# Kernel tuning notes

Measured on AMD Instinct MI355X. Metric: run time of the kernel, lower is better.

## Reference

```python
import jax, jax.numpy as jnp
import numpy as np

NEG_SLOPE = 0.2  # PyG GATConv LeakyReLU slope
HEADS = 4

def _gat_conv(x, edge_index, W, a_src, a_dst, b):
    """Single-relation GATConv (PyG semantics, concat=True).
    x: [N, Fin]; edge_index: [2, E]; W: [Fin, H*D]; a_src/a_dst: [H, D]; b: [H*D].
    """
    N = x.shape[0]
    H, D = a_src.shape
    h = (x @ W).reshape(N, H, D)                      # [N, H, D]
    src, dst = edge_index[0], edge_index[1]
    # per-node attention halves
    al_s = jnp.einsum('nhd,hd->nh', h, a_src)         # [N, H]
    al_d = jnp.einsum('nhd,hd->nh', h, a_dst)         # [N, H]
    alpha = jax.nn.leaky_relu(al_s[src] + al_d[dst], NEG_SLOPE)  # [E, H]
    # segment softmax over incoming edges per destination node
    amax = jax.ops.segment_max(alpha, dst, num_segments=N)       # [N, H]
    e = jnp.exp(alpha - amax[dst])
    denom = jax.ops.segment_sum(e, dst, num_segments=N)          # [N, H]
    w = e / (denom[dst] + 1e-16)                                  # [E, H]
    msg = h[src] * w[:, :, None]                                  # [E, H, D]
    out = jax.ops.segment_sum(msg, dst, num_segments=N)          # [N, H, D]
    return out.reshape(N, H * D) + b

def setup_inputs() -> dict:
    key = jax.random.key(0)
    ks = jax.random.split(key, 8)
    N, Fin, Fout, E, R = 50000, 256, 128, 800000, 3
    return {
        'x': jax.random.normal(ks[0], (N, Fin), dtype=jnp.float32),
        'edge_index_0': jax.random.randint(ks[1], (2, E), 0, N, dtype=jnp.int32),
        'edge_index_1': jax.random.randint(ks[2], (2, E), 0, N, dtype=jnp.int32),
        'edge_index_2': jax.random.randint(ks[3], (2, E), 0, N, dtype=jnp.int32),
        'W': jax.random.normal(ks[4], (R, Fin, Fout), dtype=jnp.float32) * 0.05,
        'att_src': jax.random.normal(ks[5], (R, HEADS, Fout // HEADS), dtype=jnp.float32) * 0.1,
        'att_dst': jax.random.normal(ks[6], (R, HEADS, Fout // HEADS), dtype=jnp.float32) * 0.1,
        'bias': jax.random.normal(ks[7], (R, Fout), dtype=jnp.float32) * 0.01,
    }

def reference(x, edge_index_0, edge_index_1, edge_index_2, W, att_src, att_dst, bias):
    edges = (edge_index_0, edge_index_1, edge_index_2)
    out = None
    for r in range(W.shape[0]):  # small fixed relation loop
        h_rel = _gat_conv(x, edges[r], W[r], att_src[r], att_dst[r], bias[r])
        out = h_rel if out is None else out + h_rel
    return out
```

## Files before the change

kernel.cpp:

```cpp
#include <hip/hip_runtime.h>
#include <hip/hip_bf16.h>

#define NEG_SLOPE 0.2f
#define NBMAX 320
#define KB    512
#define CAP   10240
#define CHUNK 4096

typedef short bf16x8 __attribute__((ext_vector_type(8)));
typedef float f32x4  __attribute__((ext_vector_type(4)));
typedef float f32x16 __attribute__((ext_vector_type(16)));

__device__ inline ushort f2bf(float f) {
  __hip_bfloat16 b = __float2bfloat16(f);
  return *(ushort*)&b;
}

__global__ __launch_bounds__(256)
void prep_kernel(const float* __restrict__ W,
                 const float* __restrict__ a_src,
                 const float* __restrict__ a_dst,
                 ushort* __restrict__ WbigT,
                 int* __restrict__ bcnt) {
  const int b = blockIdx.x;
  const int t = threadIdx.x;
  if (b == 448) {
    for (int k = t; k < NBMAX; k += 256) bcnt[k] = 0;
    return;
  }
  int i = b * 256 + t;
  int c = i >> 8, k = i & 255;
  float v = 0.f;
  if (c < 384) {
    int r = c >> 7, j = c & 127;
    v = W[((size_t)r * 256 + k) * 128 + j];
  } else if (c < 408) {
    int c6 = c - 384, r = c6 >> 3, hh = c6 & 7, hd = hh & 3;
    const float* a = (hh < 4 ? a_src : a_dst) + (r * 4 + hd) * 32;
    const float* wp = W + ((size_t)r * 256 + k) * 128 + hd * 32;
#pragma unroll
    for (int d = 0; d < 32; ++d) v += wp[d] * a[d];
  }
  WbigT[i] = f2bf(v);
}

__device__ inline void edge_decode(int i, int E0, int E1,
                                   const int* __restrict__ s0, const int* __restrict__ d0,
                                   const int* __restrict__ s1, const int* __restrict__ d1,
                                   const int* __restrict__ s2, const int* __restrict__ d2,
                                   int N, int& src, int& key) {
  if (i < E0)            { src = s0[i];            key = d0[i]; }
  else if (i < E0 + E1)  { src = s1[i - E0];       key = N + d1[i - E0]; }
  else                   { src = s2[i - E0 - E1];  key = 2 * N + d2[i - E0 - E1]; }
}

struct GemmSmem {
  ushort As[64][40];
  ushort Bs[448][40];
};
struct StageSmem {
  ushort es_src[CHUNK];
  int    es_key[CHUNK];
  int    lh[NBMAX];
  int    lb[NBMAX];
};

__global__ __launch_bounds__(256, 2)
void gemm_stage_kernel(const float* __restrict__ x, const ushort* __restrict__ WT,
                       ushort* __restrict__ hall, float* __restrict__ al, int M,
                       const int* __restrict__ s0, const int* __restrict__ d0,
                       const int* __restrict__ s1, const int* __restrict__ d1,
                       const int* __restrict__ s2, const int* __restrict__ d2,
                       int E0, int E1, int E2,
                       int* __restrict__ bcnt, unsigned* __restrict__ staging,
                       int N, int NB, int GB) {
  __shared__ __align__(16) char smem_raw[sizeof(GemmSmem) > sizeof(StageSmem)
                                             ? sizeof(GemmSmem) : sizeof(StageSmem)];
  const int t = threadIdx.x;

  if (blockIdx.x < GB) {
    GemmSmem& sm = *reinterpret_cast<GemmSmem*>(smem_raw);
    const int bm = blockIdx.x * 64;
    const int l = t & 63;
    const int w = t >> 6;
    const int wm = (w >> 1) * 32;
    const int wn = (w & 1) * 224;
    const int lr31 = l & 31;
    const int kg = (l >> 5) * 8;

    f32x16 acc[7];
#pragma unroll
    for (int j = 0; j < 7; ++j)
#pragma unroll
      for (int r = 0; r < 16; ++r) acc[j][r] = 0.f;

    for (int k0 = 0; k0 < 256; k0 += 32) {
      {
        int row = t >> 2, seg = t & 3;
        int grow = bm + row;
        float4 v0 = make_float4(0.f, 0.f, 0.f, 0.f), v1 = v0;
        if (grow < M) {
          const float* xp = x + (size_t)grow * 256 + k0 + seg * 8;
          v0 = *(const float4*)xp;
          v1 = *(const float4*)(xp + 4);
        }
        uint4 pk;
        pk.x = (unsigned)f2bf(v0.x) | ((unsigned)f2bf(v0.y) << 16);
        pk.y = (unsigned)f2bf(v0.z) | ((unsigned)f2bf(v0.w) << 16);
        pk.z = (unsigned)f2bf(v1.x) | ((unsigned)f2bf(v1.y) << 16);
        pk.w = (unsigned)f2bf(v1.z) | ((unsigned)f2bf(v1.w) << 16);
        *(uint4*)&sm.As[row][seg * 8] = pk;
      }
#pragma unroll
      for (int p = 0; p < 7; ++p) {
        int idx = p * 256 + t;
        int nrow = idx >> 2, ch = idx & 3;
        *(uint4*)&sm.Bs[nrow][ch * 8] =
            *(const uint4*)(WT + (size_t)nrow * 256 + k0 + ch * 8);
      }
      __syncthreads();
#pragma unroll
      for (int kk = 0; kk < 32; kk += 16) {
        bf16x8 af = *(bf16x8*)&sm.As[wm + lr31][kk + kg];
#pragma unroll
        for (int j = 0; j < 7; ++j) {
          bf16x8 bf = *(bf16x8*)&sm.Bs[wn + j * 32 + lr31][kk + kg];
          acc[j] = __builtin_amdgcn_mfma_f32_32x32x16_bf16(af, bf, acc[j], 0, 0, 0);
        }
      }
      __syncthreads();
    }

#pragma unroll
    for (int j = 0; j < 7; ++j) {
      int gcol = wn + j * 32 + lr31;
#pragma unroll
      for (int r = 0; r < 16; ++r) {
        int grow = bm + wm + (l >> 5) * 4 + (r & 3) + 8 * (r >> 2);
        if (grow >= M) continue;
        float c = acc[j][r];
        if (gcol < 384) {
          int rel = gcol >> 7, jj = gcol & 127;
          hall[((size_t)rel * M + grow) * 128 + jj] = f2bf(c);
        } else if (gcol < 408) {
          int c6 = gcol - 384, rr = c6 >> 3, hh = c6 & 7;
          al[(((size_t)(hh < 4 ? 0 : 3) + rr) * M + grow) * 4 + (hh & 3)] = c;
        }
      }
    }
  } else {
    StageSmem& sm = *reinterpret_cast<StageSmem*>(smem_raw);
    for (int k = t; k < NB; k += 256) sm.lh[k] = 0;
    __syncthreads();
    const int Etot = E0 + E1 + E2;
    const int lo = (blockIdx.x - GB) * CHUNK;
    const int hi = min(lo + CHUNK, Etot);
    const int n = hi - lo;
    for (int i = t; i < n; i += 256) {
      int src, key;
      edge_decode(lo + i, E0, E1, s0, d0, s1, d1, s2, d2, N, src, key);
      sm.es_src[i] = (ushort)src;
      sm.es_key[i] = key;
      atomicAdd(&sm.lh[key >> 9], 1);
    }
    __syncthreads();
    for (int k = t; k < NB; k += 256) {
      int v = sm.lh[k];
      sm.lb[k] = v ? (k * CAP + atomicAdd(&bcnt[k], v)) : 0;
      sm.lh[k] = 0;
    }
    __syncthreads();
    for (int i = t; i < n; i += 256) {
      int key = sm.es_key[i];
      int b = key >> 9;
      int pos = sm.lb[b] + atomicAdd(&sm.lh[b], 1);
      if (pos < (b + 1) * CAP)
        staging[pos] = ((unsigned)(key & 511) << 16) | (unsigned)sm.es_src[i];
    }
  }
}

__global__ __launch_bounds__(512)
void bucket_sort(const unsigned* __restrict__ staging, const int* __restrict__ bcnt,
                 int* __restrict__ offs, int* __restrict__ ends,
                 ushort* __restrict__ srt, int n3) {
  __shared__ int cnt[KB];
  __shared__ int cur[KB];
  __shared__ int wsum[8];
  const int b = blockIdx.x;
  const int base = b * KB;
  const int lo = b * CAP;
  const int t = threadIdx.x;
  const int lane = t & 63, wid = t >> 6;
  const int m = min(bcnt[b], CAP);
  cnt[t] = 0;
  __syncthreads();
  for (int i = t; i < m; i += 512)
    atomicAdd(&cnt[staging[lo + i] >> 16], 1);
  __syncthreads();
  int v = cnt[t];
  int sv = v;
#pragma unroll
  for (int d = 1; d < 64; d <<= 1) {
    int u = __shfl_up(sv, d);
    if (lane >= d) sv += u;
  }
  if (lane == 63) wsum[wid] = sv;
  __syncthreads();
  if (t < 8) {
    int ws = wsum[t];
#pragma unroll
    for (int d = 1; d < 8; d <<= 1) {
      int u = __shfl_up(ws, d);
      if (t >= d) ws += u;
    }
    wsum[t] = ws;
  }
  __syncthreads();
  int start = lo + (wid ? wsum[wid - 1] : 0) + sv - v;
  cur[t] = start;
  if (base + t < n3) {
    offs[base + t] = start;
    ends[base + t] = start + v;
  }
  __syncthreads();
  for (int i = t; i < m; i += 512) {
    unsigned p = staging[lo + i];
    int pos = atomicAdd(&cur[p >> 16], 1);
    srt[pos] = (ushort)(p & 0xffffu);
  }
}

__global__ __launch_bounds__(128)
void gat_fused_kernel(const ushort* __restrict__ srt, const int* __restrict__ offs,
                      const int* __restrict__ ends,
                      const ushort* __restrict__ hall,
                      const float* __restrict__ al,
                      const float* __restrict__ bias,
                      float* __restrict__ out, int N) {
  const int d = blockIdx.x;
  const int t = threadIdx.x;
  const int w = t >> 6;
  const int l = t & 63;
  const int eg = l >> 4;
  const int fl = l & 15;
  const int h = fl >> 2;

  __shared__ float slab[3][2][16][9];

#pragma unroll
  for (int rel = 0; rel < 3; ++rel) {
    const int key = rel * N + d;
    const int start = offs[key];
    const int dend = ends[key];
    const float* alS = al + (size_t)rel * N * 4;
    const ushort* hrel = hall + (size_t)rel * N * 128;
    const float ald = al[((size_t)(3 + rel) * N + d) * 4 + h];
    float r0 = 0.f, r1 = 0.f, r2 = 0.f, r3 = 0.f;
    float r4 = 0.f, r5 = 0.f, r6 = 0.f, r7 = 0.f;
    float dl = 0.f;
#pragma unroll 2
    for (int e = start + w * 4 + eg; e < dend; e += 8) {
      int s = srt[e];
      float a = alS[(size_t)s * 4 + h] + ald;
      a = fmaxf(a, NEG_SLOPE * a);
      float ex = __expf(a);
      dl += ex;
      uint4 u = *(const uint4*)(hrel + (size_t)s * 128 + fl * 8);
      r0 += __uint_as_float(u.x << 16) * ex;
      r1 += __uint_as_float(u.x & 0xffff0000u) * ex;
      r2 += __uint_as_float(u.y << 16) * ex;
      r3 += __uint_as_float(u.y & 0xffff0000u) * ex;
      r4 += __uint_as_float(u.z << 16) * ex;
      r5 += __uint_as_float(u.z & 0xffff0000u) * ex;
      r6 += __uint_as_float(u.w << 16) * ex;
      r7 += __uint_as_float(u.w & 0xffff0000u) * ex;
    }
    r0 += __shfl_xor(r0, 16); r0 += __shfl_xor(r0, 32);
    r1 += __shfl_xor(r1, 16); r1 += __shfl_xor(r1, 32);
    r2 += __shfl_xor(r2, 16); r2 += __shfl_xor(r2, 32);
    r3 += __shfl_xor(r3, 16); r3 += __shfl_xor(r3, 32);
    r4 += __shfl_xor(r4, 16); r4 += __shfl_xor(r4, 32);
    r5 += __shfl_xor(r5, 16); r5 += __shfl_xor(r5, 32);
    r6 += __shfl_xor(r6, 16); r6 += __shfl_xor(r6, 32);
    r7 += __shfl_xor(r7, 16); r7 += __shfl_xor(r7, 32);
    dl += __shfl_xor(dl, 16); dl += __shfl_xor(dl, 32);
    if (l < 16) {
      slab[rel][w][fl][0] = r0; slab[rel][w][fl][1] = r1;
      slab[rel][w][fl][2] = r2; slab[rel][w][fl][3] = r3;
      slab[rel][w][fl][4] = r4; slab[rel][w][fl][5] = r5;
      slab[rel][w][fl][6] = r6; slab[rel][w][fl][7] = r7;
      slab[rel][w][fl][8] = dl;
    }
  }
  __syncthreads();
  {
    int fl2 = t >> 3, k = t & 7;
    int f = fl2 * 8 + k;
    float o = bias[f] + bias[128 + f] + bias[256 + f];
#pragma unroll
    for (int rel = 0; rel < 3; ++rel) {
      float D = slab[rel][0][fl2][8] + slab[rel][1][fl2][8];
      float R = slab[rel][0][fl2][k] + slab[rel][1][fl2][k];
      o += R / (D + 1e-16f);
    }
    out[(size_t)d * 128 + f] = o;
  }
}

extern "C" void kernel_launch(void* const* d_in, const int* in_sizes, int n_in,
                              void* d_out, int out_size, void* d_ws, size_t ws_size,
                              hipStream_t stream) {
  const float* x     = (const float*)d_in[0];
  const int*   ei[3] = {(const int*)d_in[1], (const int*)d_in[2], (const int*)d_in[3]};
  const float* W     = (const float*)d_in[4];
  const float* a_src = (const float*)d_in[5];
  const float* a_dst = (const float*)d_in[6];
  const float* bias  = (const float*)d_in[7];

  const int Fin = 256;
  const int N = in_sizes[0] / Fin;
  const int E0 = in_sizes[1] / 2, E1 = in_sizes[2] / 2, E2 = in_sizes[3] / 2;
  const int Etot = E0 + E1 + E2;
  const int n3 = 3 * N;
  const int NB = (n3 + KB - 1) / KB;
  const int GB = (N + 63) / 64;
  const int SB = (Etot + CHUNK - 1) / CHUNK;

  float* out = (float*)d_out;

  char* p = (char*)d_ws;
  ushort*   WbigT   = (ushort*)p;    p += (size_t)448 * 256 * 2;
  ushort*   hall    = (ushort*)p;    p += (size_t)N * 384 * 2;
  float*    al      = (float*)p;     p += (size_t)6 * N * 4 * 4;
  unsigned* staging = (unsigned*)p;  p += (size_t)NBMAX * CAP * 4;
  ushort*   srt     = (ushort*)p;    p += (size_t)NBMAX * CAP * 2;
  int*      offs    = (int*)p;       p += (size_t)n3 * 4;
  int*      ends    = (int*)p;       p += (size_t)n3 * 4;
  int*      bcnt    = (int*)p;       p += NBMAX * 4;

  prep_kernel<<<449, 256, 0, stream>>>(W, a_src, a_dst, WbigT, bcnt);

  gemm_stage_kernel<<<GB + SB, 256, 0, stream>>>(
      x, WbigT, hall, al, N,
      ei[0], ei[0] + E0, ei[1], ei[1] + E1, ei[2], ei[2] + E2,
      E0, E1, E2, bcnt, staging, N, NB, GB);

  bucket_sort<<<NB, 512, 0, stream>>>(staging, bcnt, offs, ends, srt, n3);

  gat_fused_kernel<<<N, 128, 0, stream>>>(srt, offs, ends, hall, al, bias, out, N);
}
```

Baseline: 199.6 us.

## Regroup kernels: fuse edge staging with weight prep, bucket sort with GEMM

After: 198.9 us (median of 2 runs). Within noise of the previous version (-0.4%).

```diff
diff --git a/kernel.cpp b/kernel.cpp
--- a/kernel.cpp
+++ b/kernel.cpp
@@ -8,40 +8,11 @@
 #define CHUNK 4096
 
 typedef short bf16x8 __attribute__((ext_vector_type(8)));
-typedef float f32x4  __attribute__((ext_vector_type(4)));
 typedef float f32x16 __attribute__((ext_vector_type(16)));
 
 __device__ inline ushort f2bf(float f) {
   __hip_bfloat16 b = __float2bfloat16(f);
   return *(ushort*)&b;
-}
-
-__global__ __launch_bounds__(256)
-void prep_kernel(const float* __restrict__ W,
-                 const float* __restrict__ a_src,
-                 const float* __restrict__ a_dst,
-                 ushort* __restrict__ WbigT,
-                 int* __restrict__ bcnt) {
-  const int b = blockIdx.x;
-  const int t = threadIdx.x;
-  if (b == 448) {
-    for (int k = t; k < NBMAX; k += 256) bcnt[k] = 0;
-    return;
-  }
-  int i = b * 256 + t;
-  int c = i >> 8, k = i & 255;
-  float v = 0.f;
-  if (c < 384) {
-    int r = c >> 7, j = c & 127;
-    v = W[((size_t)r * 256 + k) * 128 + j];
-  } else if (c < 408) {
-    int c6 = c - 384, r = c6 >> 3, hh = c6 & 7, hd = hh & 3;
-    const float* a = (hh < 4 ? a_src : a_dst) + (r * 4 + hd) * 32;
-    const float* wp = W + ((size_t)r * 256 + k) * 128 + hd * 32;
-#pragma unroll
-    for (int d = 0; d < 32; ++d) v += wp[d] * a[d];
-  }
-  WbigT[i] = f2bf(v);
 }
 
 __device__ inline void edge_decode(int i, int E0, int E1,
@@ -54,10 +25,6 @@
   else                   { src = s2[i - E0 - E1];  key = 2 * N + d2[i - E0 - E1]; }
 }
 
-struct GemmSmem {
-  ushort As[64][40];
-  ushort Bs[448][40];
-};
 struct StageSmem {
   ushort es_src[CHUNK];
   int    es_key[CHUNK];
@@ -66,21 +33,144 @@
 };
 
 __global__ __launch_bounds__(256, 2)
-void gemm_stage_kernel(const float* __restrict__ x, const ushort* __restrict__ WT,
-                       ushort* __restrict__ hall, float* __restrict__ al, int M,
-                       const int* __restrict__ s0, const int* __restrict__ d0,
+void stage_prep_kernel(const int* __restrict__ s0, const int* __restrict__ d0,
                        const int* __restrict__ s1, const int* __restrict__ d1,
                        const int* __restrict__ s2, const int* __restrict__ d2,
                        int E0, int E1, int E2,
                        int* __restrict__ bcnt, unsigned* __restrict__ staging,
-                       int N, int NB, int GB) {
-  __shared__ __align__(16) char smem_raw[sizeof(GemmSmem) > sizeof(StageSmem)
-                                             ? sizeof(GemmSmem) : sizeof(StageSmem)];
+                       int N, int NB, int SB,
+                       const float* __restrict__ W,
+                       const float* __restrict__ a_src,
+                       const float* __restrict__ a_dst,
+                       ushort* __restrict__ WbigT) {
+  __shared__ __align__(16) char smem_raw[sizeof(StageSmem)];
   const int t = threadIdx.x;
-
-  if (blockIdx.x < GB) {
+  if (blockIdx.x >= SB) {
+    int i = (blockIdx.x - SB) * 256 + t;
+    int c = i >> 8, k = i & 255;
+    float v = 0.f;
+    if (c < 384) {
+      int r = c >> 7, j = c & 127;
+      v = W[((size_t)r * 256 + k) * 128 + j];
+    } else if (c < 408) {
+      int c6 = c - 384, r = c6 >> 3, hh = c6 & 7, hd = hh & 3;
+      const float* a = (hh < 4 ? a_src : a_dst) + (r * 4 + hd) * 32;
+      const float* wp = W + ((size_t)r * 256 + k) * 128 + hd * 32;
+#pragma unroll
+      for (int d = 0; d < 32; ++d) v += wp[d] * a[d];
+    }
+    WbigT[i] = f2bf(v);
+    return;
+  }
+  StageSmem& sm = *reinterpret_cast<StageSmem*>(smem_raw);
+  for (int k = t; k < NB; k += 256) sm.lh[k] = 0;
+  __syncthreads();
+  const int Etot = E0 + E1 + E2;
+  const int lo = blockIdx.x * CHUNK;
+  const int hi = min(lo + CHUNK, Etot);
+  const int n = hi - lo;
+  for (int i = t; i < n; i += 256) {
+    int src, key;
+    edge_decode(lo + i, E0, E1, s0, d0, s1, d1, s2, d2, N, src, key);
+    sm.es_src[i] = (ushort)src;
+    sm.es_key[i] = key;
+    atomicAdd(&sm.lh[key >> 9], 1);
+  }
+  __syncthreads();
+  for (int k = t; k < NB; k += 256) {
+    int v = sm.lh[k];
+    sm.lb[k] = v ? (k * CAP + atomicAdd(&bcnt[k], v)) : 0;
+    sm.lh[k] = 0;
+  }
+  __syncthreads();
+  for (int i = t; i < n; i += 256) {
+    int key = sm.es_key[i];
+    int b = key >> 9;
+    int pos = sm.lb[b] + atomicAdd(&sm.lh[b], 1);
+    if (pos < (b + 1) * CAP)
+      staging[pos] = ((unsigned)(key & 511) << 16) | (unsigned)sm.es_src[i];
+  }
+}
+
+struct GemmSmem {
+  ushort As[64][40];
+  ushort Bs[448][40];
+};
+struct SortSmem {
+  unsigned es[CAP];
+  int cnt[KB];
+  int cur[KB];
+  int wsum[4];
+};
+
+__global__ __launch_bounds__(256, 2)
+void sort_gemm_kernel(const unsigned* __restrict__ staging, const int* __restrict__ bcnt,
+                      int* __restrict__ offs, int* __restrict__ ends,
+                      ushort* __restrict__ srt, int n3, int NB,
+                      const float* __restrict__ x, const ushort* __restrict__ WT,
+                      ushort* __restrict__ hall, float* __restrict__ al, int M) {
+  __shared__ __align__(16) char smem_raw[sizeof(SortSmem) > sizeof(GemmSmem)
+                                             ? sizeof(SortSmem) : sizeof(GemmSmem)];
+  const int t = threadIdx.x;
+
+  if (blockIdx.x < NB) {
+    SortSmem& sm = *reinterpret_cast<SortSmem*>(smem_raw);
+    const int b = blockIdx.x;
+    const int base = b * KB;
+    const int lo = b * CAP;
+    const int m = min(bcnt[b], CAP);
+    sm.cnt[t] = 0;
+    sm.cnt[t + 256] = 0;
+    __syncthreads();
+    for (int i = t; i < m; i += 256) {
+      unsigned p = staging[lo + i];
+      sm.es[i] = p;
+      atomicAdd(&sm.cnt[p >> 16], 1);
+    }
+    __syncthreads();
+    const int lane = t & 63, wid = t >> 6;
+    int c0 = sm.cnt[2 * t], c1 = sm.cnt[2 * t + 1];
+    int v = c0 + c1;
+    int sv = v;
+#pragma unroll
+    for (int d = 1; d < 64; d <<= 1) {
+      int u = __shfl_up(sv, d);
+      if (lane >= d) sv += u;
+    }
+    if (lane == 63) sm.wsum[wid] = sv;
+    __syncthreads();
+    if (t < 4) {
+      int ws = sm.wsum[t];
+#pragma unroll
+      for (int d = 1; d < 4; d <<= 1) {
+        int u = __shfl_up(ws, d);
+        if (t >= d) ws += u;
+      }
+      sm.wsum[t] = ws;
+    }
+    __syncthreads();
+    int excl = (wid ? sm.wsum[wid - 1] : 0) + sv - v;
+    int st0 = lo + excl;
+    int st1 = st0 + c0;
+    sm.cur[2 * t] = st0;
+    sm.cur[2 * t + 1] = st1;
+    if (base + 2 * t < n3) {
+      offs[base + 2 * t] = st0;
+      ends[base + 2 * t] = st0 + c0;
+    }
+    if (base + 2 * t + 1 < n3) {
+      offs[base + 2 * t + 1] = st1;
+      ends[base + 2 * t + 1] = st1 + c1;
+    }
+    __syncthreads();
+    for (int i = t; i < m; i += 256) {
+      unsigned p = sm.es[i];
+      int pos = atomicAdd(&sm.cur[p >> 16], 1);
+      srt[pos] = (ushort)(p & 0xffffu);
+    }
+  } else {
     GemmSmem& sm = *reinterpret_cast<GemmSmem*>(smem_raw);
-    const int bm = blockIdx.x * 64;
+    const int bm = (blockIdx.x - NB) * 64;
     const int l = t & 63;
     const int w = t >> 6;
     const int wm = (w >> 1) * 32;
@@ -148,86 +238,6 @@
         }
       }
     }
-  } else {
-    StageSmem& sm = *reinterpret_cast<StageSmem*>(smem_raw);
-    for (int k = t; k < NB; k += 256) sm.lh[k] = 0;
-    __syncthreads();
-    const int Etot = E0 + E1 + E2;
-    const int lo = (blockIdx.x - GB) * CHUNK;
-    const int hi = min(lo + CHUNK, Etot);
-    const int n = hi - lo;
-    for (int i = t; i < n; i += 256) {
-      int src, key;
-      edge_decode(lo + i, E0, E1, s0, d0, s1, d1, s2, d2, N, src, key);
-      sm.es_src[i] = (ushort)src;
-      sm.es_key[i] = key;
-      atomicAdd(&sm.lh[key >> 9], 1);
-    }
-    __syncthreads();
-    for (int k = t; k < NB; k += 256) {
-      int v = sm.lh[k];
-      sm.lb[k] = v ? (k * CAP + atomicAdd(&bcnt[k], v)) : 0;
-      sm.lh[k] = 0;
-    }
-    __syncthreads();
-    for (int i = t; i < n; i += 256) {
-      int key = sm.es_key[i];
-      int b = key >> 9;
-      int pos = sm.lb[b] + atomicAdd(&sm.lh[b], 1);
-      if (pos < (b + 1) * CAP)
-        staging[pos] = ((unsigned)(key & 511) << 16) | (unsigned)sm.es_src[i];
-    }
-  }
-}
-
-__global__ __launch_bounds__(512)
-void bucket_sort(const unsigned* __restrict__ staging, const int* __restrict__ bcnt,
-                 int* __restrict__ offs, int* __restrict__ ends,
-                 ushort* __restrict__ srt, int n3) {
-  __shared__ int cnt[KB];
-  __shared__ int cur[KB];
-  __shared__ int wsum[8];
-  const int b = blockIdx.x;
-  const int base = b * KB;
-  const int lo = b * CAP;
-  const int t = threadIdx.x;
-  const int lane = t & 63, wid = t >> 6;
-  const int m = min(bcnt[b], CAP);
-  cnt[t] = 0;
-  __syncthreads();
-  for (int i = t; i < m; i += 512)
-    atomicAdd(&cnt[staging[lo + i] >> 16], 1);
-  __syncthreads();
-  int v = cnt[t];
-  int sv = v;
-#pragma unroll
-  for (int d = 1; d < 64; d <<= 1) {
-    int u = __shfl_up(sv, d);
-    if (lane >= d) sv += u;
-  }
-  if (lane == 63) wsum[wid] = sv;
-  __syncthreads();
-  if (t < 8) {
-    int ws = wsum[t];
-#pragma unroll
-    for (int d = 1; d < 8; d <<= 1) {
-      int u = __shfl_up(ws, d);
-      if (t >= d) ws += u;
-    }
-    wsum[t] = ws;
-  }
-  __syncthreads();
-  int start = lo + (wid ? wsum[wid - 1] : 0) + sv - v;
-  cur[t] = start;
-  if (base + t < n3) {
-    offs[base + t] = start;
-    ends[base + t] = start + v;
-  }
-  __syncthreads();
-  for (int i = t; i < m; i += 512) {
-    unsigned p = staging[lo + i];
-    int pos = atomicAdd(&cur[p >> 16], 1);
-    srt[pos] = (ushort)(p & 0xffffu);
   }
 }
 
@@ -339,14 +349,16 @@
   int*      ends    = (int*)p;       p += (size_t)n3 * 4;
   int*      bcnt    = (int*)p;       p += NBMAX * 4;
 
-  prep_kernel<<<449, 256, 0, stream>>>(W, a_src, a_dst, WbigT, bcnt);
-
-  gemm_stage_kernel<<<GB + SB, 256, 0, stream>>>(
-      x, WbigT, hall, al, N,
+  hipMemsetAsync(bcnt, 0, NBMAX * sizeof(int), stream);
+
+  stage_prep_kernel<<<SB + 448, 256, 0, stream>>>(
       ei[0], ei[0] + E0, ei[1], ei[1] + E1, ei[2], ei[2] + E2,
-      E0, E1, E2, bcnt, staging, N, NB, GB);
-
-  bucket_sort<<<NB, 512, 0, stream>>>(staging, bcnt, offs, ends, srt, n3);
+      E0, E1, E2, bcnt, staging, N, NB, SB,
+      W, a_src, a_dst, WbigT);
+
+  sort_gemm_kernel<<<NB + GB, 256, 0, stream>>>(
+      staging, bcnt, offs, ends, srt, n3, NB,
+      x, WbigT, hall, al, N);
 
   gat_fused_kernel<<<N, 128, 0, stream>>>(srt, offs, ends, hall, al, bias, out, N);
 }
```
